# Kernel optimization log

Hardware: AMD Instinct MI355X
Metric: run time of the kernel (lower is better)

The kernel has to match this reference:

```python
import jax, jax.numpy as jnp
import numpy as np

H = 1024
HEADS = 16
FFN = 4096
EPS = 1e-5


def _layernorm(x, g, b):
    mu = jnp.mean(x, axis=-1, keepdims=True)
    var = jnp.mean((x - mu) ** 2, axis=-1, keepdims=True)
    return (x - mu) * jax.lax.rsqrt(var + EPS) * g + b


def setup_inputs() -> dict:
    key = jax.random.key(0)
    ks = jax.random.split(key, 12)
    N, L = 2, 2048
    s = 1.0 / np.sqrt(H)
    inp = {
        "src_hidden": jax.random.normal(ks[0], (N, L, H), dtype=jnp.float32),
        "key_mask": jnp.ones((N, L), dtype=jnp.int32),
        "Wq": jax.random.normal(ks[1], (H, H), dtype=jnp.float32) * s,
        "bq": jnp.zeros((H,), dtype=jnp.float32),
        "Wk": jax.random.normal(ks[2], (H, H), dtype=jnp.float32) * s,
        "bk": jnp.zeros((H,), dtype=jnp.float32),
        "Wv": jax.random.normal(ks[3], (H, H), dtype=jnp.float32) * s,
        "bv": jnp.zeros((H,), dtype=jnp.float32),
        "Wo": jax.random.normal(ks[4], (H, H), dtype=jnp.float32) * s,
        "bo": jnp.zeros((H,), dtype=jnp.float32),
        "ln1_g": jnp.ones((H,), dtype=jnp.float32),
        "ln1_b": jnp.zeros((H,), dtype=jnp.float32),
        "W1": jax.random.normal(ks[5], (H, FFN), dtype=jnp.float32) * s,
        "b1": jnp.zeros((FFN,), dtype=jnp.float32),
        "W2": jax.random.normal(ks[6], (FFN, H), dtype=jnp.float32) * (1.0 / np.sqrt(FFN)),
        "b2": jnp.zeros((H,), dtype=jnp.float32),
        "ln2_g": jnp.ones((H,), dtype=jnp.float32),
        "ln2_b": jnp.zeros((H,), dtype=jnp.float32),
    }
    return inp


def reference(src_hidden, key_mask, Wq, bq, Wk, bk, Wv, bv, Wo, bo,
              ln1_g, ln1_b, W1, b1, W2, b2, ln2_g, ln2_b):
    N, L, _ = src_hidden.shape
    d = H // HEADS
    # projections -> (N, heads, L, d)
    q = (src_hidden @ Wq + bq).reshape(N, L, HEADS, d).transpose(0, 2, 1, 3)
    k = (src_hidden @ Wk + bk).reshape(N, L, HEADS, d).transpose(0, 2, 1, 3)
    v = (src_hidden @ Wv + bv).reshape(N, L, HEADS, d).transpose(0, 2, 1, 3)
    # faithful quirk: Q/=sqrt(H) and K/=sqrt(H)  =>  scores scaled by 1/H
    sims = jnp.einsum('bhid,bhjd->bhij', q, k) / H  # (N, heads, L, L)
    mask = key_mask[:, None, None, :] != 0          # (N,1,1,L), masked=False
    sims = jnp.where(mask, sims, -jnp.inf)
    attn = jax.nn.softmax(sims, axis=-1)
    ctx = jnp.einsum('bhij,bhjd->bhid', attn, v)
    concats = ctx.transpose(0, 2, 1, 3).reshape(N, L, H)
    mhsa = concats @ Wo + bo
    # residual + LN1
    x = _layernorm(mhsa + src_hidden, ln1_g, ln1_b)
    # FFN (dropout=0 / eval) + residual + LN2
    ffn = jax.nn.relu(x @ W1 + b1) @ W2 + b2
    out = _layernorm(ffn + x, ln2_g, ln2_b)
    return out
```

## Files before the change

kernel.cpp:

```cpp
#include <hip/hip_runtime.h>
#include <math.h>

#define Hd   1024
#define SEQL 2048
#define NB   2
#define NHEADS 16
#define FFND 4096
#define ROWS 4096
#define QKVLD 3072

typedef __attribute__((ext_vector_type(8))) short short8;
typedef __attribute__((ext_vector_type(4))) float f32x4;

__device__ __forceinline__ unsigned short f2bf(float f) {
  union { float f; unsigned int u; } v; v.f = f;
  return (unsigned short)((v.u + 0x7fffu + ((v.u >> 16) & 1u)) >> 16);
}
__device__ __forceinline__ unsigned short f2bf_fast(float f) {
  union { float f; unsigned int u; } v; v.f = f;
  return (unsigned short)((v.u + 0x8000u) >> 16);
}
__device__ __forceinline__ float bf2f(unsigned short u) {
  union { unsigned int u; float f; } v; v.u = (unsigned int)u << 16;
  return v.f;
}

__device__ __forceinline__ void gl_lds16(const unsigned short* g,
                                         unsigned short* l) {
  __builtin_amdgcn_global_load_lds(
      (const __attribute__((address_space(1))) void*)g,
      (__attribute__((address_space(3))) void*)l, 16, 0, 0);
}

__global__ __launch_bounds__(256) void convert_bf16(
    const float* __restrict__ in, unsigned short* __restrict__ out) {
  const int i = (blockIdx.x * 256 + threadIdx.x) * 4;
  float4 x = *(const float4*)&in[i];
  ushort4 o;
  o.x = f2bf(x.x); o.y = f2bf(x.y); o.z = f2bf(x.z); o.w = f2bf(x.w);
  *(ushort4*)&out[i] = o;
}

__global__ __launch_bounds__(256) void convert_transpose(
    const float* __restrict__ W, int ld,
    unsigned short* __restrict__ Wt, int ldt) {
  __shared__ float T[64][65];
  const int t = threadIdx.x;
  const int c0 = blockIdx.x * 64, r0 = blockIdx.y * 64;
#pragma unroll
  for (int p = 0; p < 4; ++p) {
    const int lin = t + p * 256;
    const int r = lin >> 4, c4 = (lin & 15) * 4;
    float4 x = *(const float4*)&W[(size_t)(r0 + r) * ld + c0 + c4];
    T[r][c4 + 0] = x.x; T[r][c4 + 1] = x.y;
    T[r][c4 + 2] = x.z; T[r][c4 + 3] = x.w;
  }
  __syncthreads();
#pragma unroll
  for (int p = 0; p < 2; ++p) {
    const int lin = t + p * 256;
    const int oc = lin >> 3, ch = (lin & 7) * 8;
    union { unsigned short u[8]; uint4 v; } x;
#pragma unroll
    for (int i = 0; i < 8; ++i) x.u[i] = f2bf(T[ch + i][oc]);
    *(uint4*)&Wt[(size_t)(c0 + oc) * ldt + r0 + ch] = x.v;
  }
}

__global__ __launch_bounds__(256) void convert_transpose4(
    const float* __restrict__ W0, const float* __restrict__ W1,
    const float* __restrict__ W2, const float* __restrict__ W3,
    unsigned short* __restrict__ T0, unsigned short* __restrict__ T1,
    unsigned short* __restrict__ T2, unsigned short* __restrict__ T3) {
  __shared__ float T[64][65];
  const float* W = (blockIdx.z == 0) ? W0 : (blockIdx.z == 1) ? W1
                 : (blockIdx.z == 2) ? W2 : W3;
  unsigned short* Wt = (blockIdx.z == 0) ? T0 : (blockIdx.z == 1) ? T1
                     : (blockIdx.z == 2) ? T2 : T3;
  const int t = threadIdx.x;
  const int c0 = blockIdx.x * 64, r0 = blockIdx.y * 64;
#pragma unroll
  for (int p = 0; p < 4; ++p) {
    const int lin = t + p * 256;
    const int r = lin >> 4, c4 = (lin & 15) * 4;
    float4 x = *(const float4*)&W[(size_t)(r0 + r) * Hd + c0 + c4];
    T[r][c4 + 0] = x.x; T[r][c4 + 1] = x.y;
    T[r][c4 + 2] = x.z; T[r][c4 + 3] = x.w;
  }
  __syncthreads();
#pragma unroll
  for (int p = 0; p < 2; ++p) {
    const int lin = t + p * 256;
    const int oc = lin >> 3, ch = (lin & 7) * 8;
    union { unsigned short u[8]; uint4 v; } x;
#pragma unroll
    for (int i = 0; i < 8; ++i) x.u[i] = f2bf(T[ch + i][oc]);
    *(uint4*)&Wt[(size_t)(c0 + oc) * Hd + r0 + ch] = x.v;
  }
}

__global__ __launch_bounds__(256) void concat3(
    const float* __restrict__ a, const float* __restrict__ b,
    const float* __restrict__ c, float* __restrict__ o) {
  const int i = blockIdx.x * 256 + threadIdx.x;
  o[i] = (i < 1024) ? a[i] : (i < 2048 ? b[i - 1024] : c[i - 2048]);
}

__global__ __launch_bounds__(256) void transpose_v(
    const unsigned short* __restrict__ v, unsigned short* __restrict__ vt) {
  __shared__ unsigned short T[64][72];
  const int t = threadIdx.x;
  const int s0 = (blockIdx.x & 31) * 64;
  const int bh = blockIdx.x >> 5;
  const int b = bh >> 4, h = bh & 15;
#pragma unroll
  for (int p = 0; p < 2; ++p) {
    const int lin = t + p * 256;
    const int r = lin >> 3, c8 = (lin & 7) * 8;
    *(uint4*)&T[r][c8] =
        *(const uint4*)&v[(size_t)(b * SEQL + s0 + r) * QKVLD + h * 64 + c8];
  }
  __syncthreads();
#pragma unroll
  for (int p = 0; p < 2; ++p) {
    const int lin = t + p * 256;
    const int d = lin >> 3, c8 = (lin & 7) * 8;
    union { unsigned short u[8]; uint4 v4; } x;
#pragma unroll
    for (int i = 0; i < 8; ++i) x.u[i] = T[c8 + i][d];
    *(uint4*)&vt[(size_t)(bh * 64 + d) * SEQL + s0 + c8] = x.v4;
  }
}

template <int BN, int MODE, int OUTBF>
__global__ __launch_bounds__(256, (BN == 128 ? 3 : 4)) void gemm_bt(
    const unsigned short* __restrict__ A, int lda,
    const unsigned short* __restrict__ Bt, int ldb,
    const float* __restrict__ bias,
    void* __restrict__ Cv, int ldc, int K) {
  constexpr int NI = (BN == 128) ? 4 : 2;
  __shared__ unsigned short As[128 * 32];
  __shared__ unsigned short Bs[BN * 32];
  const int t = threadIdx.x;
  const int wave = t >> 6, lane = t & 63;
  const int l16 = lane & 15, quad = lane >> 4;
  const int m0 = blockIdx.y * 128, n0 = blockIdx.x * BN;
  const int wm = (wave >> 1) * 64, wn = (wave & 1) * (BN / 2);
  const int srow = wave * 16 + (lane >> 2);
  const int scol = (lane & 3) * 8;

  f32x4 acc[4][NI];
#pragma unroll
  for (int i = 0; i < 4; ++i)
#pragma unroll
    for (int j = 0; j < NI; ++j) acc[i][j] = (f32x4){0.f, 0.f, 0.f, 0.f};

  const unsigned short* Ap0 = &A[(size_t)(m0 + srow) * lda + scol];
  const unsigned short* Ap1 = &A[(size_t)(m0 + 64 + srow) * lda + scol];
  const unsigned short* Bp0 = &Bt[(size_t)(n0 + srow) * ldb + scol];
  const unsigned short* Bp1 =
      (BN == 128) ? &Bt[(size_t)(n0 + 64 + srow) * ldb + scol] : Bp0;
  unsigned short* lA0 = &As[(wave * 16) * 32];
  unsigned short* lA1 = &As[(64 + wave * 16) * 32];
  unsigned short* lB0 = &Bs[(wave * 16) * 32];
  unsigned short* lB1 = (BN == 128) ? &Bs[(64 + wave * 16) * 32] : lB0;

  for (int k0 = 0; k0 < K; k0 += 32) {
    gl_lds16(Ap0 + k0, lA0);
    gl_lds16(Ap1 + k0, lA1);
    gl_lds16(Bp0 + k0, lB0);
    if (BN == 128) gl_lds16(Bp1 + k0, lB1);
    __syncthreads();

    short8 af[4], bfr[NI];
#pragma unroll
    for (int mi = 0; mi < 4; ++mi)
      af[mi] = *(const short8*)&As[(wm + mi * 16 + l16) * 32 + quad * 8];
#pragma unroll
    for (int ni = 0; ni < NI; ++ni)
      bfr[ni] = *(const short8*)&Bs[(wn + ni * 16 + l16) * 32 + quad * 8];
#pragma unroll
    for (int mi = 0; mi < 4; ++mi)
#pragma unroll
      for (int ni = 0; ni < NI; ++ni)
        acc[mi][ni] = __builtin_amdgcn_mfma_f32_16x16x32_bf16(
            af[mi], bfr[ni], acc[mi][ni], 0, 0, 0);
    __syncthreads();
  }

#pragma unroll
  for (int mi = 0; mi < 4; ++mi) {
#pragma unroll
    for (int ni = 0; ni < NI; ++ni) {
      const int col = n0 + wn + ni * 16 + l16;
      const float bv = (MODE == 2) ? 0.0f : bias[col];
#pragma unroll
      for (int r = 0; r < 4; ++r) {
        const int row = m0 + wm + mi * 16 + quad * 4 + r;
        float v = acc[mi][ni][r] + bv;
        if (MODE == 1) v = fmaxf(v, 0.0f);
        if (OUTBF) {
          ((unsigned short*)Cv)[(size_t)row * ldc + col] = f2bf_fast(v);
        } else {
          float* Cf = (float*)Cv;
          if (MODE == 2) Cf[(size_t)row * ldc + col] += v;
          else           Cf[(size_t)row * ldc + col] = v;
        }
      }
    }
  }
}

__global__ __launch_bounds__(256, 5) void attn_mfma(
    const unsigned short* __restrict__ Q,
    const unsigned short* __restrict__ K,
    const unsigned short* __restrict__ Vt,
    const int* __restrict__ mask,
    unsigned short* __restrict__ Op,
    float* __restrict__ ls) {
  __shared__ unsigned short Qs[64 * 72];
  __shared__ unsigned short Ks[64 * 72];
  __shared__ unsigned short Vs[64 * 72];
  unsigned short* Ps = Qs;

  const int t = threadIdx.x;
  const int wave = t >> 6, lane = t & 63;
  const int l16 = lane & 15, quad = lane >> 4;
  const int qb = blockIdx.x & 31;
  const int h  = (blockIdx.x >> 5) & 15;
  const int b  = (blockIdx.x >> 9) & 1;
  const int jh = blockIdx.x >> 10;
  const int q0 = qb * 64;
  const int bh = b * NHEADS + h;
  const int jbeg = jh * (SEQL / 2), jend = jbeg + SEQL / 2;
  const float NEGINF = -__builtin_inff();

  const int lr = t >> 3, lc8 = (t & 7) * 8;
  const unsigned short* Kbase = &K[(size_t)(b * SEQL + lr) * QKVLD + h * 64 + lc8];
  const unsigned short* Vbase = &Vt[(size_t)(bh * 64 + lr) * SEQL + lc8];
  const size_t Krow32 = (size_t)32 * QKVLD;

#pragma unroll
  for (int p = 0; p < 2; ++p) {
    const int r = lr + p * 32;
    *(uint4*)&Qs[r * 72 + lc8] =
        *(const uint4*)&Q[(size_t)(b * SEQL + q0 + r) * QKVLD + h * 64 + lc8];
  }
  __syncthreads();
  const short8 aq0 = *(const short8*)&Qs[(wave * 16 + l16) * 72 + quad * 8];
  const short8 aq1 = *(const short8*)&Qs[(wave * 16 + l16) * 72 + 32 + quad * 8];

  float lrow[4] = {0.f, 0.f, 0.f, 0.f};
  f32x4 accO[4];
#pragma unroll
  for (int nd = 0; nd < 4; ++nd) accO[nd] = (f32x4){0.f, 0.f, 0.f, 0.f};

  uint4 kv0 = *(const uint4*)(Kbase + (size_t)jbeg * QKVLD);
  uint4 kv1 = *(const uint4*)(Kbase + (size_t)jbeg * QKVLD + Krow32);
  uint4 vv0 = *(const uint4*)(Vbase + jbeg);
  uint4 vv1 = *(const uint4*)(Vbase + jbeg + 32 * SEQL);

  for (int j0 = jbeg; j0 < jend; j0 += 64) {
    __syncthreads();
    *(uint4*)&Ks[lr * 72 + lc8] = kv0;
    *(uint4*)&Ks[(lr + 32) * 72 + lc8] = kv1;
    *(uint4*)&Vs[lr * 72 + lc8] = vv0;
    *(uint4*)&Vs[(lr + 32) * 72 + lc8] = vv1;
    __syncthreads();

    if (j0 + 64 < jend) {
      const unsigned short* kp = Kbase + (size_t)(j0 + 64) * QKVLD;
      const unsigned short* vp = Vbase + (j0 + 64);
      kv0 = *(const uint4*)(kp);
      kv1 = *(const uint4*)(kp + Krow32);
      vv0 = *(const uint4*)(vp);
      vv1 = *(const uint4*)(vp + 32 * SEQL);
    }

#pragma unroll
    for (int nt = 0; nt < 4; ++nt) {
      short8 bk0 = *(const short8*)&Ks[(nt * 16 + l16) * 72 + quad * 8];
      short8 bk1 = *(const short8*)&Ks[(nt * 16 + l16) * 72 + 32 + quad * 8];
      f32x4 z = (f32x4){0.f, 0.f, 0.f, 0.f};
      z = __builtin_amdgcn_mfma_f32_16x16x32_bf16(aq0, bk0, z, 0, 0, 0);
      z = __builtin_amdgcn_mfma_f32_16x16x32_bf16(aq1, bk1, z, 0, 0, 0);
      const bool ok = mask[b * SEQL + j0 + nt * 16 + l16] != 0;
      unsigned short pk[4];
#pragma unroll
      for (int r = 0; r < 4; ++r) {
        const float x = ok ? z[r] * (1.0f / 1024.0f) : NEGINF;
        const float p = __expf(x);
        lrow[r] += p;
        pk[r] = f2bf_fast(p);
      }
#pragma unroll
      for (int r = 0; r < 4; ++r)
        Ps[(wave * 16 + quad * 4 + r) * 72 + nt * 16 + l16] = pk[r];
    }

    short8 ap0 = *(const short8*)&Ps[(wave * 16 + l16) * 72 + quad * 8];
    short8 ap1 = *(const short8*)&Ps[(wave * 16 + l16) * 72 + 32 + quad * 8];
#pragma unroll
    for (int nd = 0; nd < 4; ++nd) {
      short8 bv0 = *(const short8*)&Vs[(nd * 16 + l16) * 72 + quad * 8];
      short8 bv1 = *(const short8*)&Vs[(nd * 16 + l16) * 72 + 32 + quad * 8];
      accO[nd] = __builtin_amdgcn_mfma_f32_16x16x32_bf16(ap0, bv0, accO[nd], 0, 0, 0);
      accO[nd] = __builtin_amdgcn_mfma_f32_16x16x32_bf16(ap1, bv1, accO[nd], 0, 0, 0);
    }
  }

#pragma unroll
  for (int r = 0; r < 4; ++r) {
#pragma unroll
    for (int off = 1; off < 16; off <<= 1)
      lrow[r] += __shfl_xor(lrow[r], off, 64);
  }
  if (l16 == 0) {
#pragma unroll
    for (int r = 0; r < 4; ++r)
      ls[((size_t)(jh * NB + b) * NHEADS + h) * SEQL + q0 + wave * 16 +
         quad * 4 + r] = lrow[r];
  }
#pragma unroll
  for (int nd = 0; nd < 4; ++nd)
#pragma unroll
    for (int r = 0; r < 4; ++r) {
      const int rowg = b * SEQL + q0 + wave * 16 + quad * 4 + r;
      Op[(size_t)jh * ROWS * Hd + (size_t)rowg * Hd + h * 64 + nd * 16 + l16] =
          f2bf_fast(accO[nd][r]);
    }
}

__global__ __launch_bounds__(256) void attn_combine(
    const unsigned short* __restrict__ Op, const float* __restrict__ ls,
    unsigned short* __restrict__ ctxb) {
  const int row = blockIdx.x;
  const int b = row >> 11, q = row & (SEQL - 1);
  const int t = threadIdx.x;
  const int c0 = t * 4, h = t >> 4;
  const float l0 = ls[((size_t)(b)*NHEADS + h) * SEQL + q];
  const float l1 = ls[((size_t)(NB + b) * NHEADS + h) * SEQL + q];
  const float inv = 1.0f / (l0 + l1);
  ushort4 a = *(const ushort4*)&Op[(size_t)row * Hd + c0];
  ushort4 c = *(const ushort4*)&Op[(size_t)ROWS * Hd + (size_t)row * Hd + c0];
  ushort4 o;
  o.x = f2bf_fast((bf2f(a.x) + bf2f(c.x)) * inv);
  o.y = f2bf_fast((bf2f(a.y) + bf2f(c.y)) * inv);
  o.z = f2bf_fast((bf2f(a.z) + bf2f(c.z)) * inv);
  o.w = f2bf_fast((bf2f(a.w) + bf2f(c.w)) * inv);
  *(ushort4*)&ctxb[(size_t)row * Hd + c0] = o;
}

template <int ABF>
__global__ __launch_bounds__(256) void add_ln_kernel(
    const void* Av, const float* R,
    const float* __restrict__ gamma, const float* __restrict__ beta,
    float* out, unsigned short* outb) {
  const int row = blockIdx.x;
  const int t = threadIdx.x;
  const size_t baser = (size_t)row * Hd;

  float a0, a1, a2, a3;
  if (ABF) {
    ushort4 a = *(const ushort4*)&((const unsigned short*)Av)[baser + t * 4];
    a0 = bf2f(a.x); a1 = bf2f(a.y); a2 = bf2f(a.z); a3 = bf2f(a.w);
  } else {
    float4 a = *(const float4*)&((const float*)Av)[baser + t * 4];
    a0 = a.x; a1 = a.y; a2 = a.z; a3 = a.w;
  }
  float4 r = *(const float4*)&R[baser + t * 4];
  float x0 = a0 + r.x, x1 = a1 + r.y, x2 = a2 + r.z, x3 = a3 + r.w;
  float s  = x0 + x1 + x2 + x3;
  float ss = x0 * x0 + x1 * x1 + x2 * x2 + x3 * x3;

#pragma unroll
  for (int off = 32; off > 0; off >>= 1) {
    s  += __shfl_down(s, off, 64);
    ss += __shfl_down(ss, off, 64);
  }

  __shared__ float rs[4], rss[4];
  __shared__ float sh_mean, sh_rstd;
  if ((t & 63) == 0) { rs[t >> 6] = s; rss[t >> 6] = ss; }
  __syncthreads();
  if (t == 0) {
    const float S  = rs[0] + rs[1] + rs[2] + rs[3];
    const float SS = rss[0] + rss[1] + rss[2] + rss[3];
    const float mean = S * (1.0f / Hd);
    const float var  = SS * (1.0f / Hd) - mean * mean;
    sh_mean = mean;
    sh_rstd = rsqrtf(var + 1e-5f);
  }
  __syncthreads();
  const float mean = sh_mean, rstd = sh_rstd;

  float4 gm = *(const float4*)&gamma[t * 4];
  float4 bt = *(const float4*)&beta[t * 4];
  float4 o;
  o.x = (x0 - mean) * rstd * gm.x + bt.x;
  o.y = (x1 - mean) * rstd * gm.y + bt.y;
  o.z = (x2 - mean) * rstd * gm.z + bt.z;
  o.w = (x3 - mean) * rstd * gm.w + bt.w;
  *(float4*)&out[baser + t * 4] = o;
  if (outb) {
    ushort4 ob;
    ob.x = f2bf(o.x); ob.y = f2bf(o.y); ob.z = f2bf(o.z); ob.w = f2bf(o.w);
    *(ushort4*)&outb[baser + t * 4] = ob;
  }
}

extern "C" void kernel_launch(void* const* d_in, const int* in_sizes, int n_in,
                              void* d_out, int out_size, void* d_ws, size_t ws_size,
                              hipStream_t stream) {
  const float* src  = (const float*)d_in[0];
  const int*   kmsk = (const int*)  d_in[1];
  const float* Wq   = (const float*)d_in[2];
  const float* bq   = (const float*)d_in[3];
  const float* Wk   = (const float*)d_in[4];
  const float* bk   = (const float*)d_in[5];
  const float* Wv   = (const float*)d_in[6];
  const float* bv   = (const float*)d_in[7];
  const float* Wo   = (const float*)d_in[8];
  const float* bo   = (const float*)d_in[9];
  const float* ln1g = (const float*)d_in[10];
  const float* ln1b = (const float*)d_in[11];
  const float* W1   = (const float*)d_in[12];
  const float* b1   = (const float*)d_in[13];
  const float* W2   = (const float*)d_in[14];
  const float* b2   = (const float*)d_in[15];
  const float* ln2g = (const float*)d_in[16];
  const float* ln2b = (const float*)d_in[17];

  char* w8 = (char*)d_ws;
  char* o8 = (char*)d_out;
  const size_t MB = 1024 * 1024;
  unsigned short* srcb  = (unsigned short*)(w8 + 0 * MB);
  unsigned short* WqkvT = (unsigned short*)(w8 + 8 * MB);
  float*          bqkv  = (float*)(w8 + 14 * MB);
  unsigned short* qkv   = (unsigned short*)(w8 + 16 * MB);
  unsigned short* vt    = (unsigned short*)(w8 + 40 * MB);
  unsigned short* Opart = (unsigned short*)(w8 + 0 * MB);
  float*          ls    = (float*)(o8 + 8 * MB);
  unsigned short* WoT   = (unsigned short*)(o8 + 9 * MB);
  unsigned short* ctxb  = (unsigned short*)d_out;
  float*          mhsa  = (float*)(w8 + 16 * MB);
  float*          x1    = (float*)d_out;
  unsigned short* x1b   = (unsigned short*)(w8 + 8 * MB);
  unsigned short* W1T   = (unsigned short*)(w8 + 0 * MB);
  unsigned short* hb    = (unsigned short*)(w8 + 16 * MB);
  unsigned short* W2T   = (unsigned short*)(w8 + 0 * MB);
  unsigned short* f2b   = (unsigned short*)(w8 + 8 * MB);

  dim3 blk(256);

  convert_bf16<<<ROWS * Hd / 1024, blk, 0, stream>>>(src, srcb);
  convert_transpose4<<<dim3(16, 16, 4), blk, 0, stream>>>(
      Wq, Wk, Wv, Wo, WqkvT, WqkvT + 1024 * 1024, WqkvT + 2 * 1024 * 1024, WoT);
  concat3<<<12, blk, 0, stream>>>(bq, bk, bv, bqkv);

  gemm_bt<128, 0, 1><<<dim3(QKVLD / 128, ROWS / 128), blk, 0, stream>>>(
      srcb, Hd, WqkvT, Hd, bqkv, qkv, QKVLD, Hd);

  transpose_v<<<1024, blk, 0, stream>>>(qkv + 2048, vt);
  attn_mfma<<<2048, blk, 0, stream>>>(qkv, qkv + 1024, vt, kmsk, Opart, ls);
  attn_combine<<<ROWS, blk, 0, stream>>>(Opart, ls, ctxb);

  gemm_bt<64, 0, 0><<<dim3(Hd / 64, ROWS / 128), blk, 0, stream>>>(
      ctxb, Hd, WoT, Hd, bo, mhsa, Hd, Hd);

  add_ln_kernel<0><<<ROWS, blk, 0, stream>>>(mhsa, src, ln1g, ln1b, x1, x1b);

  convert_transpose<<<dim3(64, 16), blk, 0, stream>>>(W1, FFND, W1T, Hd);
  gemm_bt<128, 1, 1><<<dim3(FFND / 128, ROWS / 128), blk, 0, stream>>>(
      x1b, Hd, W1T, Hd, b1, hb, FFND, Hd);
  convert_transpose<<<dim3(16, 64), blk, 0, stream>>>(W2, Hd, W2T, FFND);
  gemm_bt<64, 0, 1><<<dim3(Hd / 64, ROWS / 128), blk, 0, stream>>>(
      hb, FFND, W2T, FFND, b2, f2b, Hd, FFND);

  add_ln_kernel<1><<<ROWS, blk, 0, stream>>>(f2b, x1, ln2g, ln2b,
                                             (float*)d_out, nullptr);
}
```

Before: 401.6 us.

## Restructure attention kernel: register P via shuffles, swizzled double-buffered K/V LDS

The attention kernel now computes S transposed (K as the A operand), so each lane holds probabilities for one query row. It repacks them into the PV MFMA operand with cross-lane shuffles instead of a round trip through shared memory. K/V tiles move to double-buffered, XOR-swizzled LDS without padding, which removes one barrier per iteration. Q is loaded straight from global into registers, masks are read as int4, and s_setprio wraps the MFMA sections. These changes aim to cut LDS traffic, bank conflicts and syncs, at the cost of many extra shuffle instructions.

```diff
diff --git a/kernel.cpp b/kernel.cpp
--- a/kernel.cpp
+++ b/kernel.cpp
@@ -23,6 +23,12 @@
 __device__ __forceinline__ float bf2f(unsigned short u) {
   union { unsigned int u; float f; } v; v.u = (unsigned int)u << 16;
   return v.f;
+}
+__device__ __forceinline__ int pack2bf(float lo, float hi) {
+  return (int)f2bf_fast(lo) | ((int)f2bf_fast(hi) << 16);
+}
+__device__ __forceinline__ int swz(int r, int c) {
+  return ((r << 6) | c) ^ ((r & 7) << 3);
 }
 
 __device__ __forceinline__ void gl_lds16(const unsigned short* g,
@@ -218,10 +224,8 @@
     const int* __restrict__ mask,
     unsigned short* __restrict__ Op,
     float* __restrict__ ls) {
-  __shared__ unsigned short Qs[64 * 72];
-  __shared__ unsigned short Ks[64 * 72];
-  __shared__ unsigned short Vs[64 * 72];
-  unsigned short* Ps = Qs;
+  __shared__ unsigned short Ks[2][64 * 64];
+  __shared__ unsigned short Vs[2][64 * 64];
 
   const int t = threadIdx.x;
   const int wave = t >> 6, lane = t & 63;
@@ -240,17 +244,12 @@
   const unsigned short* Vbase = &Vt[(size_t)(bh * 64 + lr) * SEQL + lc8];
   const size_t Krow32 = (size_t)32 * QKVLD;
 
-#pragma unroll
-  for (int p = 0; p < 2; ++p) {
-    const int r = lr + p * 32;
-    *(uint4*)&Qs[r * 72 + lc8] =
-        *(const uint4*)&Q[(size_t)(b * SEQL + q0 + r) * QKVLD + h * 64 + lc8];
-  }
-  __syncthreads();
-  const short8 aq0 = *(const short8*)&Qs[(wave * 16 + l16) * 72 + quad * 8];
-  const short8 aq1 = *(const short8*)&Qs[(wave * 16 + l16) * 72 + 32 + quad * 8];
-
-  float lrow[4] = {0.f, 0.f, 0.f, 0.f};
+  const unsigned short* Qrow =
+      &Q[(size_t)(b * SEQL + q0 + wave * 16 + l16) * QKVLD + h * 64];
+  const short8 aq0 = *(const short8*)&Qrow[quad * 8];
+  const short8 aq1 = *(const short8*)&Qrow[32 + quad * 8];
+
+  float lrow = 0.f;
   f32x4 accO[4];
 #pragma unroll
   for (int nd = 0; nd < 4; ++nd) accO[nd] = (f32x4){0.f, 0.f, 0.f, 0.f};
@@ -260,12 +259,18 @@
   uint4 vv0 = *(const uint4*)(Vbase + jbeg);
   uint4 vv1 = *(const uint4*)(Vbase + jbeg + 32 * SEQL);
 
+  const int srcA = l16 + ((quad & 1) << 5);
+  const int srcB = srcA + 16;
+  const bool lo2 = (quad < 2);
+
+  int cur = 0;
   for (int j0 = jbeg; j0 < jend; j0 += 64) {
-    __syncthreads();
-    *(uint4*)&Ks[lr * 72 + lc8] = kv0;
-    *(uint4*)&Ks[(lr + 32) * 72 + lc8] = kv1;
-    *(uint4*)&Vs[lr * 72 + lc8] = vv0;
-    *(uint4*)&Vs[(lr + 32) * 72 + lc8] = vv1;
+    unsigned short* Kc = Ks[cur];
+    unsigned short* Vc = Vs[cur];
+    *(uint4*)&Kc[swz(lr, lc8)] = kv0;
+    *(uint4*)&Kc[swz(lr + 32, lc8)] = kv1;
+    *(uint4*)&Vc[swz(lr, lc8)] = vv0;
+    *(uint4*)&Vc[swz(lr + 32, lc8)] = vv1;
     __syncthreads();
 
     if (j0 + 64 < jend) {
@@ -277,50 +282,63 @@
       vv1 = *(const uint4*)(vp + 32 * SEQL);
     }
 
+    int dp[4][2];
 #pragma unroll
     for (int nt = 0; nt < 4; ++nt) {
-      short8 bk0 = *(const short8*)&Ks[(nt * 16 + l16) * 72 + quad * 8];
-      short8 bk1 = *(const short8*)&Ks[(nt * 16 + l16) * 72 + 32 + quad * 8];
+      const short8 bk0 = *(const short8*)&Kc[swz(nt * 16 + l16, quad * 8)];
+      const short8 bk1 = *(const short8*)&Kc[swz(nt * 16 + l16, 32 + quad * 8)];
+      const int4 mm = *(const int4*)&mask[b * SEQL + j0 + nt * 16 + quad * 4];
       f32x4 z = (f32x4){0.f, 0.f, 0.f, 0.f};
-      z = __builtin_amdgcn_mfma_f32_16x16x32_bf16(aq0, bk0, z, 0, 0, 0);
-      z = __builtin_amdgcn_mfma_f32_16x16x32_bf16(aq1, bk1, z, 0, 0, 0);
-      const bool ok = mask[b * SEQL + j0 + nt * 16 + l16] != 0;
-      unsigned short pk[4];
+      __builtin_amdgcn_s_setprio(1);
+      z = __builtin_amdgcn_mfma_f32_16x16x32_bf16(bk0, aq0, z, 0, 0, 0);
+      z = __builtin_amdgcn_mfma_f32_16x16x32_bf16(bk1, aq1, z, 0, 0, 0);
+      __builtin_amdgcn_s_setprio(0);
+      const int mr[4] = {mm.x, mm.y, mm.z, mm.w};
+      float p[4];
 #pragma unroll
       for (int r = 0; r < 4; ++r) {
-        const float x = ok ? z[r] * (1.0f / 1024.0f) : NEGINF;
-        const float p = __expf(x);
-        lrow[r] += p;
-        pk[r] = f2bf_fast(p);
+        const float x = mr[r] ? z[r] * (1.0f / 1024.0f) : NEGINF;
+        p[r] = __expf(x);
       }
-#pragma unroll
-      for (int r = 0; r < 4; ++r)
-        Ps[(wave * 16 + quad * 4 + r) * 72 + nt * 16 + l16] = pk[r];
+      lrow += (p[0] + p[1]) + (p[2] + p[3]);
+      dp[nt][0] = pack2bf(p[0], p[1]);
+      dp[nt][1] = pack2bf(p[2], p[3]);
     }
 
-    short8 ap0 = *(const short8*)&Ps[(wave * 16 + l16) * 72 + quad * 8];
-    short8 ap1 = *(const short8*)&Ps[(wave * 16 + l16) * 72 + 32 + quad * 8];
+    union { int i[4]; short8 s; } A0, A1;
+    {
+      const int a0 = __shfl(dp[0][0], srcA), b0 = __shfl(dp[1][0], srcA);
+      const int a1 = __shfl(dp[0][1], srcA), b1 = __shfl(dp[1][1], srcA);
+      const int a2 = __shfl(dp[0][0], srcB), b2 = __shfl(dp[1][0], srcB);
+      const int a3 = __shfl(dp[0][1], srcB), b3 = __shfl(dp[1][1], srcB);
+      A0.i[0] = lo2 ? a0 : b0; A0.i[1] = lo2 ? a1 : b1;
+      A0.i[2] = lo2 ? a2 : b2; A0.i[3] = lo2 ? a3 : b3;
+      const int c0 = __shfl(dp[2][0], srcA), d0 = __shfl(dp[3][0], srcA);
+      const int c1 = __shfl(dp[2][1], srcA), d1 = __shfl(dp[3][1], srcA);
+      const int c2 = __shfl(dp[2][0], srcB), d2 = __shfl(dp[3][0], srcB);
+      const int c3 = __shfl(dp[2][1], srcB), d3 = __shfl(dp[3][1], srcB);
+      A1.i[0] = lo2 ? c0 : d0; A1.i[1] = lo2 ? c1 : d1;
+      A1.i[2] = lo2 ? c2 : d2; A1.i[3] = lo2 ? c3 : d3;
+    }
+
+    __builtin_amdgcn_s_setprio(1);
 #pragma unroll
     for (int nd = 0; nd < 4; ++nd) {
-      short8 bv0 = *(const short8*)&Vs[(nd * 16 + l16) * 72 + quad * 8];
-      short8 bv1 = *(const short8*)&Vs[(nd * 16 + l16) * 72 + 32 + quad * 8];
-      accO[nd] = __builtin_amdgcn_mfma_f32_16x16x32_bf16(ap0, bv0, accO[nd], 0, 0, 0);
-      accO[nd] = __builtin_amdgcn_mfma_f32_16x16x32_bf16(ap1, bv1, accO[nd], 0, 0, 0);
+      const short8 bv0 = *(const short8*)&Vc[swz(nd * 16 + l16, quad * 8)];
+      const short8 bv1 = *(const short8*)&Vc[swz(nd * 16 + l16, 32 + quad * 8)];
+      accO[nd] = __builtin_amdgcn_mfma_f32_16x16x32_bf16(A0.s, bv0, accO[nd], 0, 0, 0);
+      accO[nd] = __builtin_amdgcn_mfma_f32_16x16x32_bf16(A1.s, bv1, accO[nd], 0, 0, 0);
     }
-  }
-
-#pragma unroll
-  for (int r = 0; r < 4; ++r) {
-#pragma unroll
-    for (int off = 1; off < 16; off <<= 1)
-      lrow[r] += __shfl_xor(lrow[r], off, 64);
-  }
-  if (l16 == 0) {
-#pragma unroll
-    for (int r = 0; r < 4; ++r)
-      ls[((size_t)(jh * NB + b) * NHEADS + h) * SEQL + q0 + wave * 16 +
-         quad * 4 + r] = lrow[r];
-  }
+    __builtin_amdgcn_s_setprio(0);
+    cur ^= 1;
+  }
+
+  lrow += __shfl_xor(lrow, 16);
+  lrow += __shfl_xor(lrow, 32);
+  if (lane < 16)
+    ls[((size_t)(jh * NB + b) * NHEADS + h) * SEQL + q0 + wave * 16 + lane] =
+        lrow;
+
 #pragma unroll
   for (int nd = 0; nd < 4; ++nd)
 #pragma unroll
```

Result: no change. 407.5 us (+1.5%).

## Add 256x256-tile 8-wave pipelined MFMA GEMM for QKV and FFN1 projections

Applied to the files above, without the earlier changes.

Adds a new GEMM kernel with 256x256 output tiles, 512 threads, double-buffered LDS filled by direct global-to-LDS loads, XOR-swizzled layout, and interleaved barriers with priority raising around the MFMA bursts. It replaces the 128-tile gemm_bt for the QKV projection and the first FFN GEMM. The aim is more operand reuse per byte loaded and better overlap of loads with matrix math. In exchange the grid gets smaller (192 and 256 blocks), which can leave CUs underfilled, and the kernel uses 128 KB of LDS, which limits occupancy.

```diff
diff --git a/kernel.cpp b/kernel.cpp
--- a/kernel.cpp
+++ b/kernel.cpp
@@ -206,6 +206,173 @@
           if (MODE == 2) Cf[(size_t)row * ldc + col] += v;
           else           Cf[(size_t)row * ldc + col] = v;
         }
+      }
+    }
+  }
+}
+
+template <int MODE>
+__global__ __launch_bounds__(512, 2) void gemm256(
+    const unsigned short* __restrict__ A, int lda,
+    const unsigned short* __restrict__ Bt, int ldb,
+    const float* __restrict__ bias,
+    unsigned short* __restrict__ C, int ldc, int K) {
+  __shared__ unsigned short As[2][256 * 64];
+  __shared__ unsigned short Bs[2][256 * 64];
+  const int t = threadIdx.x;
+  const int wave = t >> 6, lane = t & 63;
+  const int l16 = lane & 15, quad = lane >> 4;
+  const int m0 = blockIdx.y * 256, n0 = blockIdx.x * 256;
+  const int wm = (wave >> 2) * 128, wn = (wave & 3) * 64;
+
+  const int srow = t >> 3;
+  const int scol = 8 * ((t & 7) ^ ((t >> 3) & 7));
+  const unsigned short* Ab = &A[(size_t)(m0 + srow) * lda + scol];
+  const unsigned short* Bb = &Bt[(size_t)(n0 + srow) * ldb + scol];
+
+  auto stgA = [&](int buf, int kt, int h) {
+    const unsigned short* g = Ab + (size_t)(h * 128) * lda + kt * 64;
+    unsigned short* l = &As[buf][h * 8192 + wave * 512];
+    gl_lds16(g, l);
+    gl_lds16(g + (size_t)64 * lda, l + 4096);
+  };
+  auto stgB = [&](int buf, int kt, int h) {
+    const unsigned short* g = Bb + (size_t)(h * 128) * ldb + kt * 64;
+    unsigned short* l = &Bs[buf][h * 8192 + wave * 512];
+    gl_lds16(g, l);
+    gl_lds16(g + (size_t)64 * ldb, l + 4096);
+  };
+
+  f32x4 acc[8][4];
+#pragma unroll
+  for (int i = 0; i < 8; ++i)
+#pragma unroll
+    for (int j = 0; j < 4; ++j) acc[i][j] = (f32x4){0.f, 0.f, 0.f, 0.f};
+
+  const int NT = K >> 6;
+
+  stgA(0, 0, 0); stgA(0, 0, 1);
+  stgB(0, 0, 0); stgB(0, 0, 1);
+  if (NT > 1) {
+    stgB(1, 1, 0); stgB(1, 1, 1);
+    asm volatile("s_waitcnt vmcnt(4)" ::: "memory");
+  } else {
+    asm volatile("s_waitcnt vmcnt(0)" ::: "memory");
+  }
+  __builtin_amdgcn_s_barrier();
+
+  short8 bq[4];
+  for (int tk = 0; tk < NT; ++tk) {
+    const int cb = tk & 1, nb = cb ^ 1;
+    short8 af[4];
+
+#pragma unroll
+    for (int mi = 0; mi < 4; ++mi) {
+      const int r = wm + mi * 16 + l16;
+      af[mi] = *(const short8*)&As[cb][r * 64 + ((quad * 8) ^ ((r & 7) * 8))];
+    }
+#pragma unroll
+    for (int ni = 0; ni < 4; ++ni) {
+      const int r = wn + ni * 16 + l16;
+      bq[ni] = *(const short8*)&Bs[cb][r * 64 + ((quad * 8) ^ ((r & 7) * 8))];
+    }
+    if (tk + 1 < NT) stgA(nb, tk + 1, 0);
+    __builtin_amdgcn_sched_barrier(0);
+    __builtin_amdgcn_s_barrier();
+    asm volatile("s_waitcnt lgkmcnt(0)" ::: "memory");
+    __builtin_amdgcn_sched_barrier(0);
+    __builtin_amdgcn_s_setprio(1);
+#pragma unroll
+    for (int mi = 0; mi < 4; ++mi)
+#pragma unroll
+      for (int ni = 0; ni < 4; ++ni)
+        acc[mi][ni] = __builtin_amdgcn_mfma_f32_16x16x32_bf16(
+            af[mi], bq[ni], acc[mi][ni], 0, 0, 0);
+    __builtin_amdgcn_s_setprio(0);
+    __builtin_amdgcn_s_barrier();
+
+#pragma unroll
+    for (int mi = 0; mi < 4; ++mi) {
+      const int r = wm + 64 + mi * 16 + l16;
+      af[mi] = *(const short8*)&As[cb][r * 64 + ((quad * 8) ^ ((r & 7) * 8))];
+    }
+    if (tk + 1 < NT) stgA(nb, tk + 1, 1);
+    __builtin_amdgcn_sched_barrier(0);
+    __builtin_amdgcn_s_barrier();
+    asm volatile("s_waitcnt lgkmcnt(0)" ::: "memory");
+    __builtin_amdgcn_sched_barrier(0);
+    __builtin_amdgcn_s_setprio(1);
+#pragma unroll
+    for (int mi = 0; mi < 4; ++mi)
+#pragma unroll
+      for (int ni = 0; ni < 4; ++ni)
+        acc[4 + mi][ni] = __builtin_amdgcn_mfma_f32_16x16x32_bf16(
+            af[mi], bq[ni], acc[4 + mi][ni], 0, 0, 0);
+    __builtin_amdgcn_s_setprio(0);
+    __builtin_amdgcn_s_barrier();
+
+#pragma unroll
+    for (int mi = 0; mi < 4; ++mi) {
+      const int r = wm + mi * 16 + l16;
+      af[mi] = *(const short8*)&As[cb][r * 64 + ((32 + quad * 8) ^ ((r & 7) * 8))];
+    }
+#pragma unroll
+    for (int ni = 0; ni < 4; ++ni) {
+      const int r = wn + ni * 16 + l16;
+      bq[ni] = *(const short8*)&Bs[cb][r * 64 + ((32 + quad * 8) ^ ((r & 7) * 8))];
+    }
+    __builtin_amdgcn_sched_barrier(0);
+    __builtin_amdgcn_s_barrier();
+    asm volatile("s_waitcnt lgkmcnt(0)" ::: "memory");
+    __builtin_amdgcn_sched_barrier(0);
+    __builtin_amdgcn_s_setprio(1);
+#pragma unroll
+    for (int mi = 0; mi < 4; ++mi)
+#pragma unroll
+      for (int ni = 0; ni < 4; ++ni)
+        acc[mi][ni] = __builtin_amdgcn_mfma_f32_16x16x32_bf16(
+            af[mi], bq[ni], acc[mi][ni], 0, 0, 0);
+    __builtin_amdgcn_s_setprio(0);
+    __builtin_amdgcn_s_barrier();
+
+#pragma unroll
+    for (int mi = 0; mi < 4; ++mi) {
+      const int r = wm + 64 + mi * 16 + l16;
+      af[mi] = *(const short8*)&As[cb][r * 64 + ((32 + quad * 8) ^ ((r & 7) * 8))];
+    }
+    if (tk + 2 < NT) { stgB(cb, tk + 2, 0); stgB(cb, tk + 2, 1); }
+    __builtin_amdgcn_sched_barrier(0);
+    __builtin_amdgcn_s_barrier();
+    asm volatile("s_waitcnt lgkmcnt(0)" ::: "memory");
+    __builtin_amdgcn_sched_barrier(0);
+    __builtin_amdgcn_s_setprio(1);
+#pragma unroll
+    for (int mi = 0; mi < 4; ++mi)
+#pragma unroll
+      for (int ni = 0; ni < 4; ++ni)
+        acc[4 + mi][ni] = __builtin_amdgcn_mfma_f32_16x16x32_bf16(
+            af[mi], bq[ni], acc[4 + mi][ni], 0, 0, 0);
+    __builtin_amdgcn_s_setprio(0);
+    if (tk + 2 < NT) {
+      asm volatile("s_waitcnt vmcnt(4)" ::: "memory");
+    } else if (tk + 1 < NT) {
+      asm volatile("s_waitcnt vmcnt(0)" ::: "memory");
+    }
+    __builtin_amdgcn_s_barrier();
+  }
+
+#pragma unroll
+  for (int mi = 0; mi < 8; ++mi) {
+#pragma unroll
+    for (int ni = 0; ni < 4; ++ni) {
+      const int col = n0 + wn + ni * 16 + l16;
+      const float bv = bias[col];
+#pragma unroll
+      for (int r = 0; r < 4; ++r) {
+        const int row = m0 + wm + mi * 16 + quad * 4 + r;
+        float v = acc[mi][ni][r] + bv;
+        if (MODE == 1) v = fmaxf(v, 0.0f);
+        C[(size_t)row * ldc + col] = f2bf_fast(v);
       }
     }
   }
@@ -452,13 +619,14 @@
   unsigned short* f2b   = (unsigned short*)(w8 + 8 * MB);
 
   dim3 blk(256);
+  dim3 blk8(512);
 
   convert_bf16<<<ROWS * Hd / 1024, blk, 0, stream>>>(src, srcb);
   convert_transpose4<<<dim3(16, 16, 4), blk, 0, stream>>>(
       Wq, Wk, Wv, Wo, WqkvT, WqkvT + 1024 * 1024, WqkvT + 2 * 1024 * 1024, WoT);
   concat3<<<12, blk, 0, stream>>>(bq, bk, bv, bqkv);
 
-  gemm_bt<128, 0, 1><<<dim3(QKVLD / 128, ROWS / 128), blk, 0, stream>>>(
+  gemm256<0><<<dim3(QKVLD / 256, ROWS / 256), blk8, 0, stream>>>(
       srcb, Hd, WqkvT, Hd, bqkv, qkv, QKVLD, Hd);
 
   transpose_v<<<1024, blk, 0, stream>>>(qkv + 2048, vt);
@@ -471,7 +639,7 @@
   add_ln_kernel<0><<<ROWS, blk, 0, stream>>>(mhsa, src, ln1g, ln1b, x1, x1b);
 
   convert_transpose<<<dim3(64, 16), blk, 0, stream>>>(W1, FFND, W1T, Hd);
-  gemm_bt<128, 1, 1><<<dim3(FFND / 128, ROWS / 128), blk, 0, stream>>>(
+  gemm256<1><<<dim3(FFND / 256, ROWS / 256), blk8, 0, stream>>>(
       x1b, Hd, W1T, Hd, b1, hb, FFND, Hd);
   convert_transpose<<<dim3(16, 64), blk, 0, stream>>>(W2, Hd, W2T, FFND);
   gemm_bt<64, 0, 1><<<dim3(Hd / 64, ROWS / 128), blk, 0, stream>>>(
```

After: 404.2 us. About the same (+0.6%).

## Double GEMM K-tile to 64 and XOR-swizzle LDS layout to avoid bank conflicts

Applied to the files above, without the earlier changes.

The bf16 GEMM now stages a 64-wide K slice per iteration instead of 32. That halves the number of barrier pairs and loop iterations per K and doubles the MFMA work between syncs. The shared-memory tiles use an XOR swizzle on 16-byte chunks so the wider rows do not produce LDS bank conflicts on fragment reads. LDS use per block doubles, which may lower occupancy relative to the launch bounds.

```diff
diff --git a/kernel.cpp b/kernel.cpp
--- a/kernel.cpp
+++ b/kernel.cpp
@@ -139,15 +139,17 @@
     const float* __restrict__ bias,
     void* __restrict__ Cv, int ldc, int K) {
   constexpr int NI = (BN == 128) ? 4 : 2;
-  __shared__ unsigned short As[128 * 32];
-  __shared__ unsigned short Bs[BN * 32];
+  constexpr int BG = BN / 32;
+  __shared__ unsigned short As[128 * 64];
+  __shared__ unsigned short Bs[BN * 64];
   const int t = threadIdx.x;
   const int wave = t >> 6, lane = t & 63;
   const int l16 = lane & 15, quad = lane >> 4;
   const int m0 = blockIdx.y * 128, n0 = blockIdx.x * BN;
   const int wm = (wave >> 1) * 64, wn = (wave & 1) * (BN / 2);
-  const int srow = wave * 16 + (lane >> 2);
-  const int scol = (lane & 3) * 8;
+
+  const int lr8 = lane >> 3;
+  const int sc8 = 8 * ((lane & 7) ^ lr8);
 
   f32x4 acc[4][NI];
 #pragma unroll
@@ -155,36 +157,50 @@
 #pragma unroll
     for (int j = 0; j < NI; ++j) acc[i][j] = (f32x4){0.f, 0.f, 0.f, 0.f};
 
-  const unsigned short* Ap0 = &A[(size_t)(m0 + srow) * lda + scol];
-  const unsigned short* Ap1 = &A[(size_t)(m0 + 64 + srow) * lda + scol];
-  const unsigned short* Bp0 = &Bt[(size_t)(n0 + srow) * ldb + scol];
-  const unsigned short* Bp1 =
-      (BN == 128) ? &Bt[(size_t)(n0 + 64 + srow) * ldb + scol] : Bp0;
-  unsigned short* lA0 = &As[(wave * 16) * 32];
-  unsigned short* lA1 = &As[(64 + wave * 16) * 32];
-  unsigned short* lB0 = &Bs[(wave * 16) * 32];
-  unsigned short* lB1 = (BN == 128) ? &Bs[(64 + wave * 16) * 32] : lB0;
-
-  for (int k0 = 0; k0 < K; k0 += 32) {
-    gl_lds16(Ap0 + k0, lA0);
-    gl_lds16(Ap1 + k0, lA1);
-    gl_lds16(Bp0 + k0, lB0);
-    if (BN == 128) gl_lds16(Bp1 + k0, lB1);
+  const unsigned short* Apg[4];
+  unsigned short* lAg[4];
+#pragma unroll
+  for (int j = 0; j < 4; ++j) {
+    const int r0 = (wave + 4 * j) * 8;
+    Apg[j] = &A[(size_t)(m0 + r0 + lr8) * lda + sc8];
+    lAg[j] = &As[r0 * 64];
+  }
+  const unsigned short* Bpg[BG];
+  unsigned short* lBg[BG];
+#pragma unroll
+  for (int j = 0; j < BG; ++j) {
+    const int r0 = (wave + 4 * j) * 8;
+    Bpg[j] = &Bt[(size_t)(n0 + r0 + lr8) * ldb + sc8];
+    lBg[j] = &Bs[r0 * 64];
+  }
+
+  for (int k0 = 0; k0 < K; k0 += 64) {
+#pragma unroll
+    for (int j = 0; j < 4; ++j) gl_lds16(Apg[j] + k0, lAg[j]);
+#pragma unroll
+    for (int j = 0; j < BG; ++j) gl_lds16(Bpg[j] + k0, lBg[j]);
     __syncthreads();
 
-    short8 af[4], bfr[NI];
-#pragma unroll
-    for (int mi = 0; mi < 4; ++mi)
-      af[mi] = *(const short8*)&As[(wm + mi * 16 + l16) * 32 + quad * 8];
-#pragma unroll
-    for (int ni = 0; ni < NI; ++ni)
-      bfr[ni] = *(const short8*)&Bs[(wn + ni * 16 + l16) * 32 + quad * 8];
-#pragma unroll
-    for (int mi = 0; mi < 4; ++mi)
-#pragma unroll
-      for (int ni = 0; ni < NI; ++ni)
-        acc[mi][ni] = __builtin_amdgcn_mfma_f32_16x16x32_bf16(
-            af[mi], bfr[ni], acc[mi][ni], 0, 0, 0);
+#pragma unroll
+    for (int kh = 0; kh < 2; ++kh) {
+      short8 af[4], bfr[NI];
+#pragma unroll
+      for (int mi = 0; mi < 4; ++mi) {
+        const int r = wm + mi * 16 + l16;
+        af[mi] = *(const short8*)&As[r * 64 + (((quad + 4 * kh) ^ (r & 7)) * 8)];
+      }
+#pragma unroll
+      for (int ni = 0; ni < NI; ++ni) {
+        const int r = wn + ni * 16 + l16;
+        bfr[ni] = *(const short8*)&Bs[r * 64 + (((quad + 4 * kh) ^ (r & 7)) * 8)];
+      }
+#pragma unroll
+      for (int mi = 0; mi < 4; ++mi)
+#pragma unroll
+        for (int ni = 0; ni < NI; ++ni)
+          acc[mi][ni] = __builtin_amdgcn_mfma_f32_16x16x32_bf16(
+              af[mi], bfr[ni], acc[mi][ni], 0, 0, 0);
+    }
     __syncthreads();
   }
 
```

Measured after the change: 387.4 us. 3.5% less time.
